# Kernel tuning notes

Hardware: AMD Instinct MI355X
Metric: run time of the kernel (lower is better)

The kernel has to match this reference:

```python
import jax, jax.numpy as jnp
import numpy as np

B, N, K = 2, 8192, 16
D1, D2, OUT = 128, 256, 128


def setup_inputs() -> dict:
    key = jax.random.key(0)
    ks = jax.random.split(key, 6)
    return {
        "xyz1": jax.random.normal(ks[0], (B, N, 3), dtype=jnp.float32),
        "xyz2": jax.random.normal(ks[1], (B, N, 3), dtype=jnp.float32),
        "points1": jax.random.normal(ks[2], (B, N, D1), dtype=jnp.float32),
        "points2": jax.random.normal(ks[3], (B, N, D2), dtype=jnp.float32),
        # Conv1d(k=1) == pointwise linear: weight [OUT, D1+D2], bias [OUT]
        "W": jax.random.normal(ks[4], (OUT, D1 + D2), dtype=jnp.float32) / np.sqrt(D1 + D2).astype(np.float32),
        "b": jax.random.normal(ks[5], (OUT,), dtype=jnp.float32) * 0.01,
        "nsample": K,
    }


def reference(xyz1, xyz2, points1, points2, W, b, nsample):
    Bb, Nn, _ = xyz1.shape
    # squared pairwise distances, queries=xyz2, keys=xyz1 -> [B, N, N]
    d2 = (jnp.sum(xyz2 * xyz2, -1)[:, :, None]
          + jnp.sum(xyz1 * xyz1, -1)[:, None, :]
          - 2.0 * jnp.einsum('bsc,bnc->bsn', xyz2, xyz1))
    neg_vals, idx = jax.lax.top_k(-d2, nsample)          # K nearest
    dists = -neg_vals                                     # [B, N, K] sq dists
    recip = 1.0 / (dists + 1e-8)
    weight = recip / jnp.sum(recip, axis=2, keepdims=True)  # inverse-dist weights
    # gather neighbor features from points2: [B, N, K, D2]
    g = jnp.take_along_axis(points2, idx.reshape(Bb, Nn * nsample)[:, :, None], axis=1)
    g = g.reshape(Bb, Nn, nsample, -1)
    interp = jnp.sum(g * weight[..., None], axis=2)       # [B, N, D2]
    cat = jnp.concatenate([points1, interp], axis=-1)     # [B, N, D1+D2]
    # Conv1d(kernel=1) over channel dim
    return jnp.einsum('bnc,oc->bno', cat, W) + b
```

## Files before the change

### kernel.cpp

```cpp
#include <hip/hip_runtime.h>
#include <stdint.h>

#define BQ   2
#define NQ   8192
#define D1Q  128
#define D2Q  256
#define OUTQ 128
#define CATQ 384
#define KQ   16

#define NBIN 4096
#define RED_MARGIN 1e-3f
#define LB_MARGIN  1e-2f

#define WS_WFH   0
#define WS_WFL   98304
#define WS_HIST  196608
#define WS_SPXYZ 262144
#define WS_QSXYZ 524288
#define WS_SPIDX 786432
#define WS_QSIDX 819200
#define WS_GBLO  851968
#define WS_GBHI  856064

__device__ __forceinline__ ushort f2bf(float f) {
    uint32_t u = __float_as_uint(f);
    return (ushort)((u + 0x7FFFu + ((u >> 16) & 1u)) >> 16);
}
__device__ __forceinline__ float bf2f(ushort h) {
    return __uint_as_float((uint32_t)h << 16);
}

typedef __attribute__((ext_vector_type(8))) short short8v;
typedef __attribute__((ext_vector_type(4))) float f32x4v;

__device__ __forceinline__ int mort_bin(float x, float y, float z) {
    int bx = (int)((x + 5.0f) * 1.6f); bx = bx < 0 ? 0 : (bx > 15 ? 15 : bx);
    int by = (int)((y + 5.0f) * 1.6f); by = by < 0 ? 0 : (by > 15 ? 15 : by);
    int bz = (int)((z + 5.0f) * 1.6f); bz = bz < 0 ? 0 : (bz > 15 ? 15 : bz);
    int k = 0;
    #pragma unroll
    for (int t = 0; t < 4; ++t)
        k |= (((bx >> t) & 1) << (3 * t)) | (((by >> t) & 1) << (3 * t + 1)) |
             (((bz >> t) & 1) << (3 * t + 2));
    return k;
}

__global__ void prep_w_kernel(const float* __restrict__ W,
                              ushort* __restrict__ Wfh, ushort* __restrict__ Wfl,
                              uint32_t* __restrict__ hist) {
    int flat = blockIdx.x * 256 + threadIdx.x;
    if (flat < CATQ * OUTQ) {
        int r    = flat & 7;
        int lane = (flat >> 3) & 63;
        int ctk  = flat >> 9;
        int ct   = ctk & 7;
        int kt   = ctk >> 3;
        int o = ct * 16 + (lane & 15);
        int k = kt * 32 + (lane >> 4) * 8 + r;
        float v  = W[o * CATQ + k];
        ushort h = f2bf(v);
        Wfh[flat] = h;
        Wfl[flat] = f2bf(v - bf2f(h));
    }
    if (flat < 4 * NBIN) hist[flat] = 0u;
}

__global__ void hist_kernel(const float* __restrict__ xyz1,
                            const float* __restrict__ xyz2,
                            uint32_t* __restrict__ hist) {
    int i = blockIdx.x * 256 + threadIdx.x;
    if (i < BQ * NQ) {
        int batch = i >> 13;
        const float* p = xyz1 + (size_t)i * 3;
        int bin = mort_bin(p[0], p[1], p[2]);
        atomicAdd(&hist[batch * NBIN + bin], 1u);
    } else {
        int j = i - BQ * NQ;
        int batch = j >> 13;
        const float* p = xyz2 + (size_t)j * 3;
        int bin = mort_bin(p[0], p[1], p[2]);
        atomicAdd(&hist[(2 + batch) * NBIN + bin], 1u);
    }
}

__global__ void prefix_kernel(uint32_t* __restrict__ hist) {
    __shared__ uint32_t sc[1024];
    uint32_t* h = hist + (size_t)blockIdx.x * NBIN;
    int t = threadIdx.x;
    uint32_t v0 = h[4 * t], v1 = h[4 * t + 1], v2 = h[4 * t + 2], v3 = h[4 * t + 3];
    uint32_t s = v0 + v1 + v2 + v3;
    sc[t] = s;
    __syncthreads();
    for (int d = 1; d < 1024; d <<= 1) {
        uint32_t x = (t >= d) ? sc[t - d] : 0u;
        __syncthreads();
        sc[t] += x;
        __syncthreads();
    }
    uint32_t excl = sc[t] - s;
    h[4 * t]     = excl;
    h[4 * t + 1] = excl + v0;
    h[4 * t + 2] = excl + v0 + v1;
    h[4 * t + 3] = excl + v0 + v1 + v2;
}

__global__ void scatter_kernel(const float* __restrict__ xyz1,
                               const float* __restrict__ xyz2,
                               uint32_t* __restrict__ hist,
                               float4* __restrict__ sp_xyzn,
                               float4* __restrict__ qs_xyzw,
                               ushort* __restrict__ sp_idx,
                               ushort* __restrict__ qs_idx) {
    int i = blockIdx.x * 256 + threadIdx.x;
    if (i < BQ * NQ) {
        int batch = i >> 13;
        const float* p = xyz1 + (size_t)i * 3;
        float x = p[0], y = p[1], z = p[2];
        int bin = mort_bin(x, y, z);
        uint32_t pos = atomicAdd(&hist[batch * NBIN + bin], 1u);
        float n;
        {
            #pragma clang fp contract(off)
            float px = x * x, py = y * y, pz = z * z;
            n = (px + py) + pz;
        }
        sp_xyzn[batch * NQ + pos] = make_float4(x, y, z, n);
        sp_idx[batch * NQ + pos]  = (ushort)(i & (NQ - 1));
    } else {
        int j = i - BQ * NQ;
        int batch = j >> 13;
        const float* p = xyz2 + (size_t)j * 3;
        float x = p[0], y = p[1], z = p[2];
        int bin = mort_bin(x, y, z);
        uint32_t pos = atomicAdd(&hist[(2 + batch) * NBIN + bin], 1u);
        float s2;
        {
            #pragma clang fp contract(off)
            float px = x * x, py = y * y, pz = z * z;
            s2 = (px + py) + pz;
        }
        qs_xyzw[batch * NQ + pos] = make_float4(x, y, z, s2);
        qs_idx[batch * NQ + pos]  = (ushort)(j & (NQ - 1));
    }
}

__global__ void gbox_kernel(const float4* __restrict__ sp_xyzn,
                            float4* __restrict__ gblo, float4* __restrict__ gbhi) {
    int g = blockIdx.x;
    int lane = threadIdx.x;
    float4 pt = sp_xyzn[(size_t)g * 64 + lane];
    float lx = pt.x, ly = pt.y, lz = pt.z;
    float hx = pt.x, hy = pt.y, hz = pt.z;
    #pragma unroll
    for (int d = 1; d < 64; d <<= 1) {
        lx = fminf(lx, __shfl_xor(lx, d, 64));
        ly = fminf(ly, __shfl_xor(ly, d, 64));
        lz = fminf(lz, __shfl_xor(lz, d, 64));
        hx = fmaxf(hx, __shfl_xor(hx, d, 64));
        hy = fmaxf(hy, __shfl_xor(hy, d, 64));
        hz = fmaxf(hz, __shfl_xor(hz, d, 64));
    }
    if (lane == 0) {
        gblo[g] = make_float4(lx, ly, lz, 0.f);
        gbhi[g] = make_float4(hx, hy, hz, 0.f);
    }
}

__device__ __forceinline__ float npy_d2(float4 pt, float qx, float qy, float qz,
                                        float s2) {
    #pragma clang fp contract(off)
    float d0  = pt.x * qx;
    float dot = fmaf(pt.y, qy, d0);
    dot       = fmaf(pt.z, qz, dot);
    float tt  = s2 + pt.w;
    return tt - 2.0f * dot;
}

__device__ __forceinline__ float red_r(float4 pt, float qx, float qy, float qz) {
    float dot = fmaf(pt.z, qz, fmaf(pt.y, qy, pt.x * qx));
    return fmaf(-2.0f, dot, pt.w);
}

__device__ __forceinline__ uint64_t sort64(uint64_t x, int lane) {
    #pragma unroll
    for (int k = 2; k <= 64; k <<= 1) {
        #pragma unroll
        for (int j = k >> 1; j > 0; j >>= 1) {
            uint64_t p = __shfl_xor((unsigned long long)x, j, 64);
            bool keep_min = (((lane & j) == 0) == ((lane & k) == 0));
            bool pless    = p < x;
            x = (pless == keep_min) ? p : x;
        }
    }
    return x;
}

__global__ __launch_bounds__(256, 4) void fused_kernel(
        const float4* __restrict__ sp_xyzn, const ushort* __restrict__ sp_idx,
        const float4* __restrict__ qs_xyzw, const ushort* __restrict__ qs_idx,
        const float* __restrict__ points1, const float* __restrict__ points2,
        const ushort* __restrict__ Wfh, const ushort* __restrict__ Wfl,
        const float* __restrict__ bias,
        const float4* __restrict__ gblo, const float4* __restrict__ gbhi,
        float* __restrict__ out) {
    __shared__ __align__(16) char smem[33792];
    float4*   xyzt4 = (float4*)smem;
    uint64_t* wball = (uint64_t*)(smem + 16384);
    ushort*   pidm  = (ushort*)(smem + 32768);
    ushort*   slist = (ushort*)(smem + 33280);
    ushort*   qsl   = (ushort*)(smem + 33536);
    uint32_t* scntp = (uint32_t*)(smem + 33568);
    float4*   qbl   = (float4*)(smem + 33584);
    float4*   qbh   = (float4*)(smem + 33648);
    float*    thmaxA= (float*)(smem + 33712);
    ushort*   cat_h = (ushort*)smem;
    ushort*   cat_l = (ushort*)(smem + 12544);

    const int tid   = threadIdx.x;
    const int lane  = tid & 63;
    const int w     = tid >> 6;
    const int blk   = blockIdx.x;
    const int b     = blk >> 9;
    const int qslot = (blk & 511) * 16;

    if (tid == 0) *scntp = 0u;
    if (tid < 16) qsl[tid] = qs_idx[b * NQ + qslot + tid];

    float qx[4], qy[4], qz[4], s2[4];
    int   oqi[4];
    #pragma unroll
    for (int j = 0; j < 4; ++j) {
        float4 q = qs_xyzw[(size_t)b * NQ + qslot + w * 4 + j];
        qx[j] = q.x; qy[j] = q.y; qz[j] = q.z; s2[j] = q.w;
        oqi[j] = (int)qs_idx[b * NQ + qslot + w * 4 + j];
    }
    {
        float blx = qx[0], bly = qy[0], blz = qz[0];
        float bhx = qx[0], bhy = qy[0], bhz = qz[0];
        #pragma unroll
        for (int j = 1; j < 4; ++j) {
            blx = fminf(blx, qx[j]); bly = fminf(bly, qy[j]); blz = fminf(blz, qz[j]);
            bhx = fmaxf(bhx, qx[j]); bhy = fmaxf(bhy, qy[j]); bhz = fmaxf(bhz, qz[j]);
        }
        if (lane == 0) {
            qbl[w] = make_float4(blx, bly, blz, 0.f);
            qbh[w] = make_float4(bhx, bhy, bhz, 0.f);
        }
    }

    const float4* spb = sp_xyzn + (size_t)b * NQ;
    const ushort* spi = sp_idx  + (size_t)b * NQ;

    int wstart = qslot + 8 - 1024;
    if (wstart < 0) wstart = 0;
    if (wstart > NQ - 2048) wstart = NQ - 2048;
    wstart &= ~63;

    float mn[4];
    #pragma unroll
    for (int j = 0; j < 4; ++j) mn[j] = __uint_as_float(0x7F800000u);

    for (int tile = 0; tile < 2; ++tile) {
        __syncthreads();
        {
            const float4* s4 = spb + wstart + tile * 1024;
            #pragma unroll
            for (int v = tid; v < 1024; v += 256) xyzt4[v] = s4[v];
        }
        __syncthreads();
        #pragma unroll 4
        for (int s = 0; s < 16; ++s) {
            float4 pt = xyzt4[s * 64 + lane];
            #pragma unroll
            for (int j = 0; j < 4; ++j)
                mn[j] = fminf(mn[j], red_r(pt, qx[j], qy[j], qz[j]));
        }
    }

    float that[4];
    #pragma unroll
    for (int j = 0; j < 4; ++j) {
        float x = mn[j];
        #pragma unroll
        for (int k = 2; k <= 64; k <<= 1) {
            #pragma unroll
            for (int jj = k >> 1; jj > 0; jj >>= 1) {
                float px = __shfl_xor(x, jj, 64);
                bool keep_min = (((lane & jj) == 0) == ((lane & k) == 0));
                float mnv = fminf(x, px), mxv = fmaxf(x, px);
                x = keep_min ? mnv : mxv;
            }
        }
        that[j] = s2[j] + __shfl(x, 15, 64) + RED_MARGIN;
    }
    {
        float tm = fmaxf(fmaxf(that[0], that[1]), fmaxf(that[2], that[3]));
        if (lane == 0) thmaxA[w] = tm;
    }
    __syncthreads();

    if (tid < 128) {
        float4 gl = gblo[b * 128 + tid];
        float4 gh = gbhi[b * 128 + tid];
        float qlx = fminf(fminf(qbl[0].x, qbl[1].x), fminf(qbl[2].x, qbl[3].x));
        float qly = fminf(fminf(qbl[0].y, qbl[1].y), fminf(qbl[2].y, qbl[3].y));
        float qlz = fminf(fminf(qbl[0].z, qbl[1].z), fminf(qbl[2].z, qbl[3].z));
        float qhx = fmaxf(fmaxf(qbh[0].x, qbh[1].x), fmaxf(qbh[2].x, qbh[3].x));
        float qhy = fmaxf(fmaxf(qbh[0].y, qbh[1].y), fmaxf(qbh[2].y, qbh[3].y));
        float qhz = fmaxf(fmaxf(qbh[0].z, qbh[1].z), fmaxf(qbh[2].z, qbh[3].z));
        float tmax = fmaxf(fmaxf(thmaxA[0], thmaxA[1]),
                           fmaxf(thmaxA[2], thmaxA[3]));
        float dx = fmaxf(fmaxf(qlx - gh.x, gl.x - qhx), 0.f);
        float dy = fmaxf(fmaxf(qly - gh.y, gl.y - qhy), 0.f);
        float dz = fmaxf(fmaxf(qlz - gh.z, gl.z - qhz), 0.f);
        float lb = dx * dx;
        lb = fmaf(dy, dy, lb);
        lb = fmaf(dz, dz, lb);
        if (lb <= tmax + LB_MARGIN) {
            uint32_t p = atomicAdd(scntp, 1u);
            slist[p] = (ushort)tid;
        }
    }
    __syncthreads();
    const int scnt = (int)*scntp;

    uint32_t cnt[4] = {0u, 0u, 0u, 0u};
    for (int c0 = 0; c0 < scnt; c0 += 4) {
        __syncthreads();
        {
            int which = c0 + (tid >> 6);
            if (which < scnt) {
                int off = (int)slist[which] * 64 + (tid & 63);
                xyzt4[tid] = spb[off];
                pidm[tid]  = spi[off];
            }
        }
        __syncthreads();
        const int nch = (scnt - c0) < 4 ? (scnt - c0) : 4;
        for (int k = 0; k < nch; ++k) {
            float4 pt = xyzt4[k * 64 + lane];
            #pragma unroll
            for (int j = 0; j < 4; ++j) {
                float d2 = npy_d2(pt, qx[j], qy[j], qz[j], s2[j]);
                bool  v  = (d2 <= that[j]);
                uint64_t mask = __ballot((int)v);
                if (mask != 0ull) {
                    if (v) {
                        uint32_t below = __builtin_amdgcn_mbcnt_hi(
                            (uint32_t)(mask >> 32),
                            __builtin_amdgcn_mbcnt_lo((uint32_t)mask, 0u));
                        uint32_t pos    = cnt[j] + below;
                        uint32_t bits   = __float_as_uint(d2);
                        uint32_t mapped = bits ^ (0x80000000u |
                                          (uint32_t)((int32_t)bits >> 31));
                        if (pos < 128u) {
                            uint32_t pidx = (uint32_t)pidm[k * 64 + lane];
                            wball[(w * 4 + j) * 128 + pos] =
                                ((uint64_t)mapped << 32) | (uint64_t)pidx;
                        }
                    }
                    cnt[j] += (uint32_t)__popcll(mask);
                }
            }
        }
    }

    int   myidxA[4];
    float mywgtA[4];
    #pragma unroll
    for (int j = 0; j < 4; ++j) {
        const uint64_t* wb = wball + (size_t)(w * 4 + j) * 128;
        const uint32_t c = cnt[j];
        uint64_t mykey;
        if (c <= 64u) {
            uint64_t k0 = (lane < (int)c) ? wb[lane] : ~0ull;
            mykey = sort64(k0, lane);
        } else {
            uint32_t cc = c > 128u ? 128u : c;
            uint64_t k0 = wb[lane];
            uint64_t k1 = (lane + 64 < (int)cc) ? wb[lane + 64] : ~0ull;
            k0 = sort64(k0, lane);
            k1 = sort64(k1, lane);
            uint64_t t1 = __shfl((unsigned long long)k1, lane & 15, 64);
            uint64_t km = (lane < 16) ? k0 : ((lane < 32) ? t1 : ~0ull);
            mykey = sort64(km, lane);
        }
        uint32_t mhi   = (uint32_t)(mykey >> 32);
        uint32_t rbits = (mhi & 0x80000000u) ? (mhi ^ 0x80000000u) : ~mhi;
        float    d2w   = __uint_as_float(rbits);
        myidxA[j] = (int)(uint32_t)(mykey & 0xFFFFFFFFull);
        float recip = (lane < KQ) ? (1.0f / (d2w + 1e-8f)) : 0.0f;
        float tot = recip;
        #pragma unroll
        for (int sh = 1; sh < 16; sh <<= 1) tot += __shfl_xor(tot, sh, 64);
        mywgtA[j] = recip / tot;
    }

    __syncthreads();

    const float* p2b = points2 + (size_t)b * NQ * D2Q;
    #pragma unroll
    for (int j = 0; j < 4; ++j) {
        const int qi = w * 4 + j;
        if (lane < 32) {
            float4 p = ((const float4*)(points1 +
                        (size_t)(b * NQ + oqi[j]) * D1Q))[lane];
            ushort4 hv, lv;
            hv.x = f2bf(p.x); lv.x = f2bf(p.x - bf2f(hv.x));
            hv.y = f2bf(p.y); lv.y = f2bf(p.y - bf2f(hv.y));
            hv.z = f2bf(p.z); lv.z = f2bf(p.z - bf2f(hv.z));
            hv.w = f2bf(p.w); lv.w = f2bf(p.w - bf2f(hv.w));
            *(ushort4*)&cat_h[qi * 392 + lane * 4] = hv;
            *(ushort4*)&cat_l[qi * 392 + lane * 4] = lv;
        }
        float4 acc = make_float4(0.f, 0.f, 0.f, 0.f);
        #pragma unroll
        for (int k = 0; k < KQ; ++k) {
            int   kk = __builtin_amdgcn_readlane(myidxA[j], k);
            float wk = __uint_as_float((uint32_t)__builtin_amdgcn_readlane(
                           (int)__float_as_uint(mywgtA[j]), k));
            float4 row = ((const float4*)(p2b + (size_t)kk * D2Q))[lane];
            acc.x = fmaf(wk, row.x, acc.x);
            acc.y = fmaf(wk, row.y, acc.y);
            acc.z = fmaf(wk, row.z, acc.z);
            acc.w = fmaf(wk, row.w, acc.w);
        }
        {
            ushort4 hv, lv;
            hv.x = f2bf(acc.x); lv.x = f2bf(acc.x - bf2f(hv.x));
            hv.y = f2bf(acc.y); lv.y = f2bf(acc.y - bf2f(hv.y));
            hv.z = f2bf(acc.z); lv.z = f2bf(acc.z - bf2f(hv.z));
            hv.w = f2bf(acc.w); lv.w = f2bf(acc.w - bf2f(hv.w));
            *(ushort4*)&cat_h[qi * 392 + D1Q + lane * 4] = hv;
            *(ushort4*)&cat_l[qi * 392 + D1Q + lane * 4] = lv;
        }
    }
    __syncthreads();

    {
        const int arow = lane & 15;
        const int koff = (lane >> 4) * 8;
        const int ct0  = w * 2;
        f32x4v acc0 = {0.f, 0.f, 0.f, 0.f};
        f32x4v acc1 = {0.f, 0.f, 0.f, 0.f};
        #pragma unroll 4
        for (int kt = 0; kt < 12; ++kt) {
            short8v ah = *(const short8v*)&cat_h[arow * 392 + kt * 32 + koff];
            short8v al = *(const short8v*)&cat_l[arow * 392 + kt * 32 + koff];
            const ushort* bhp = Wfh + ((size_t)(kt * 8 + ct0) * 64 + lane) * 8;
            const ushort* blp = Wfl + ((size_t)(kt * 8 + ct0) * 64 + lane) * 8;
            short8v bh0 = *(const short8v*)bhp;
            short8v bl0 = *(const short8v*)blp;
            short8v bh1 = *(const short8v*)(bhp + 512);
            short8v bl1 = *(const short8v*)(blp + 512);
            acc0 = __builtin_amdgcn_mfma_f32_16x16x32_bf16(ah, bh0, acc0, 0, 0, 0);
            acc0 = __builtin_amdgcn_mfma_f32_16x16x32_bf16(al, bh0, acc0, 0, 0, 0);
            acc0 = __builtin_amdgcn_mfma_f32_16x16x32_bf16(ah, bl0, acc0, 0, 0, 0);
            acc1 = __builtin_amdgcn_mfma_f32_16x16x32_bf16(ah, bh1, acc1, 0, 0, 0);
            acc1 = __builtin_amdgcn_mfma_f32_16x16x32_bf16(al, bh1, acc1, 0, 0, 0);
            acc1 = __builtin_amdgcn_mfma_f32_16x16x32_bf16(ah, bl1, acc1, 0, 0, 0);
        }
        const int col0   = ct0 * 16 + (lane & 15);
        const int r0slot = (lane >> 4) * 4;
        const float bv0 = bias[col0];
        const float bv1 = bias[col0 + 16];
        #pragma unroll
        for (int r = 0; r < 4; ++r) {
            int oq = (int)qsl[r0slot + r];
            size_t rowoff = (size_t)(b * NQ + oq) * OUTQ;
            out[rowoff + col0]      = acc0[r] + bv0;
            out[rowoff + col0 + 16] = acc1[r] + bv1;
        }
    }
}

extern "C" void kernel_launch(void* const* d_in, const int* in_sizes, int n_in,
                              void* d_out, int out_size, void* d_ws, size_t ws_size,
                              hipStream_t stream) {
    const float* xyz1    = (const float*)d_in[0];
    const float* xyz2    = (const float*)d_in[1];
    const float* points1 = (const float*)d_in[2];
    const float* points2 = (const float*)d_in[3];
    const float* W       = (const float*)d_in[4];
    const float* bias    = (const float*)d_in[5];

    char* ws = (char*)d_ws;
    ushort*   Wfh     = (ushort*)(ws + WS_WFH);
    ushort*   Wfl     = (ushort*)(ws + WS_WFL);
    uint32_t* hist    = (uint32_t*)(ws + WS_HIST);
    float4*   sp_xyzn = (float4*)(ws + WS_SPXYZ);
    float4*   qs_xyzw = (float4*)(ws + WS_QSXYZ);
    ushort*   sp_idx  = (ushort*)(ws + WS_SPIDX);
    ushort*   qs_idx  = (ushort*)(ws + WS_QSIDX);
    float4*   gblo    = (float4*)(ws + WS_GBLO);
    float4*   gbhi    = (float4*)(ws + WS_GBHI);

    prep_w_kernel<<<192, 256, 0, stream>>>(W, Wfh, Wfl, hist);
    hist_kernel<<<128, 256, 0, stream>>>(xyz1, xyz2, hist);
    prefix_kernel<<<4, 1024, 0, stream>>>(hist);
    scatter_kernel<<<128, 256, 0, stream>>>(xyz1, xyz2, hist,
                                            sp_xyzn, qs_xyzw, sp_idx, qs_idx);
    gbox_kernel<<<256, 64, 0, stream>>>(sp_xyzn, gblo, gbhi);
    fused_kernel<<<(BQ * NQ) / 16, 256, 0, stream>>>(
        sp_xyzn, sp_idx, qs_xyzw, qs_idx, points1, points2,
        Wfh, Wfl, bias, gblo, gbhi, (float*)d_out);
}
```

Baseline: 164.3 us.

## Fold group boxes into scatter and make kNN candidate search per-wave

```diff
diff --git a/kernel.cpp b/kernel.cpp
--- a/kernel.cpp
+++ b/kernel.cpp
@@ -20,8 +20,7 @@
 #define WS_QSXYZ 524288
 #define WS_SPIDX 786432
 #define WS_QSIDX 819200
-#define WS_GBLO  851968
-#define WS_GBHI  856064
+#define WS_GB    851968
 
 __device__ __forceinline__ ushort f2bf(float f) {
     uint32_t u = __float_as_uint(f);
@@ -29,6 +28,20 @@
 }
 __device__ __forceinline__ float bf2f(ushort h) {
     return __uint_as_float((uint32_t)h << 16);
+}
+
+__device__ __forceinline__ uint32_t encf(float f) {
+    uint32_t b = __float_as_uint(f);
+    return b ^ (0x80000000u | (uint32_t)((int32_t)b >> 31));
+}
+__device__ __forceinline__ float decf(uint32_t u) {
+    uint32_t bits = (u & 0x80000000u) ? (u ^ 0x80000000u) : ~u;
+    return __uint_as_float(bits);
+}
+
+__device__ __forceinline__ uint32_t mbcnt64(uint64_t m) {
+    return __builtin_amdgcn_mbcnt_hi((uint32_t)(m >> 32),
+           __builtin_amdgcn_mbcnt_lo((uint32_t)m, 0u));
 }
 
 typedef __attribute__((ext_vector_type(8))) short short8v;
@@ -48,7 +61,8 @@
 
 __global__ void prep_w_kernel(const float* __restrict__ W,
                               ushort* __restrict__ Wfh, ushort* __restrict__ Wfl,
-                              uint32_t* __restrict__ hist) {
+                              uint32_t* __restrict__ hist,
+                              uint32_t* __restrict__ gbU) {
     int flat = blockIdx.x * 256 + threadIdx.x;
     if (flat < CATQ * OUTQ) {
         int r    = flat & 7;
@@ -64,6 +78,7 @@
         Wfl[flat] = f2bf(v - bf2f(h));
     }
     if (flat < 4 * NBIN) hist[flat] = 0u;
+    if (flat < 256 * 8)  gbU[flat] = ((flat & 7) >= 4) ? 0u : 0xFFFFFFFFu;
 }
 
 __global__ void hist_kernel(const float* __restrict__ xyz1,
@@ -111,7 +126,8 @@
                                float4* __restrict__ sp_xyzn,
                                float4* __restrict__ qs_xyzw,
                                ushort* __restrict__ sp_idx,
-                               ushort* __restrict__ qs_idx) {
+                               ushort* __restrict__ qs_idx,
+                               uint32_t* __restrict__ gbU) {
     int i = blockIdx.x * 256 + threadIdx.x;
     if (i < BQ * NQ) {
         int batch = i >> 13;
@@ -127,6 +143,13 @@
         }
         sp_xyzn[batch * NQ + pos] = make_float4(x, y, z, n);
         sp_idx[batch * NQ + pos]  = (ushort)(i & (NQ - 1));
+        uint32_t* gw = gbU + ((size_t)batch * 128 + (pos >> 6)) * 8;
+        atomicMin(&gw[0], encf(x));
+        atomicMin(&gw[1], encf(y));
+        atomicMin(&gw[2], encf(z));
+        atomicMax(&gw[4], encf(x));
+        atomicMax(&gw[5], encf(y));
+        atomicMax(&gw[6], encf(z));
     } else {
         int j = i - BQ * NQ;
         int batch = j >> 13;
@@ -145,28 +168,6 @@
     }
 }
 
-__global__ void gbox_kernel(const float4* __restrict__ sp_xyzn,
-                            float4* __restrict__ gblo, float4* __restrict__ gbhi) {
-    int g = blockIdx.x;
-    int lane = threadIdx.x;
-    float4 pt = sp_xyzn[(size_t)g * 64 + lane];
-    float lx = pt.x, ly = pt.y, lz = pt.z;
-    float hx = pt.x, hy = pt.y, hz = pt.z;
-    #pragma unroll
-    for (int d = 1; d < 64; d <<= 1) {
-        lx = fminf(lx, __shfl_xor(lx, d, 64));
-        ly = fminf(ly, __shfl_xor(ly, d, 64));
-        lz = fminf(lz, __shfl_xor(lz, d, 64));
-        hx = fmaxf(hx, __shfl_xor(hx, d, 64));
-        hy = fmaxf(hy, __shfl_xor(hy, d, 64));
-        hz = fmaxf(hz, __shfl_xor(hz, d, 64));
-    }
-    if (lane == 0) {
-        gblo[g] = make_float4(lx, ly, lz, 0.f);
-        gbhi[g] = make_float4(hx, hy, hz, 0.f);
-    }
-}
-
 __device__ __forceinline__ float npy_d2(float4 pt, float qx, float qy, float qz,
                                         float s2) {
     #pragma clang fp contract(off)
@@ -201,21 +202,14 @@
         const float4* __restrict__ qs_xyzw, const ushort* __restrict__ qs_idx,
         const float* __restrict__ points1, const float* __restrict__ points2,
         const ushort* __restrict__ Wfh, const ushort* __restrict__ Wfl,
-        const float* __restrict__ bias,
-        const float4* __restrict__ gblo, const float4* __restrict__ gbhi,
+        const float* __restrict__ bias, const uint32_t* __restrict__ gbU,
         float* __restrict__ out) {
-    __shared__ __align__(16) char smem[33792];
-    float4*   xyzt4 = (float4*)smem;
-    uint64_t* wball = (uint64_t*)(smem + 16384);
-    ushort*   pidm  = (ushort*)(smem + 32768);
-    ushort*   slist = (ushort*)(smem + 33280);
-    ushort*   qsl   = (ushort*)(smem + 33536);
-    uint32_t* scntp = (uint32_t*)(smem + 33568);
-    float4*   qbl   = (float4*)(smem + 33584);
-    float4*   qbh   = (float4*)(smem + 33648);
-    float*    thmaxA= (float*)(smem + 33712);
+    __shared__ __align__(16) char smem[26368];
+    uint64_t* wball = (uint64_t*)smem;
     ushort*   cat_h = (ushort*)smem;
     ushort*   cat_l = (ushort*)(smem + 12544);
+    ushort*   slist = (ushort*)(smem + 25088);
+    ushort*   qsl   = (ushort*)(smem + 26112);
 
     const int tid   = threadIdx.x;
     const int lane  = tid & 63;
@@ -224,7 +218,6 @@
     const int b     = blk >> 9;
     const int qslot = (blk & 511) * 16;
 
-    if (tid == 0) *scntp = 0u;
     if (tid < 16) qsl[tid] = qs_idx[b * NQ + qslot + tid];
 
     float qx[4], qy[4], qz[4], s2[4];
@@ -235,47 +228,26 @@
         qx[j] = q.x; qy[j] = q.y; qz[j] = q.z; s2[j] = q.w;
         oqi[j] = (int)qs_idx[b * NQ + qslot + w * 4 + j];
     }
-    {
-        float blx = qx[0], bly = qy[0], blz = qz[0];
-        float bhx = qx[0], bhy = qy[0], bhz = qz[0];
-        #pragma unroll
-        for (int j = 1; j < 4; ++j) {
-            blx = fminf(blx, qx[j]); bly = fminf(bly, qy[j]); blz = fminf(blz, qz[j]);
-            bhx = fmaxf(bhx, qx[j]); bhy = fmaxf(bhy, qy[j]); bhz = fmaxf(bhz, qz[j]);
-        }
-        if (lane == 0) {
-            qbl[w] = make_float4(blx, bly, blz, 0.f);
-            qbh[w] = make_float4(bhx, bhy, bhz, 0.f);
-        }
-    }
 
     const float4* spb = sp_xyzn + (size_t)b * NQ;
     const ushort* spi = sp_idx  + (size_t)b * NQ;
 
-    int wstart = qslot + 8 - 1024;
+    int wstart = qslot + 8 - 512;
     if (wstart < 0) wstart = 0;
-    if (wstart > NQ - 2048) wstart = NQ - 2048;
+    if (wstart > NQ - 1024) wstart = NQ - 1024;
     wstart &= ~63;
+    const float4* win = spb + wstart;
 
     float mn[4];
     #pragma unroll
     for (int j = 0; j < 4; ++j) mn[j] = __uint_as_float(0x7F800000u);
 
-    for (int tile = 0; tile < 2; ++tile) {
-        __syncthreads();
-        {
-            const float4* s4 = spb + wstart + tile * 1024;
-            #pragma unroll
-            for (int v = tid; v < 1024; v += 256) xyzt4[v] = s4[v];
-        }
-        __syncthreads();
-        #pragma unroll 4
-        for (int s = 0; s < 16; ++s) {
-            float4 pt = xyzt4[s * 64 + lane];
-            #pragma unroll
-            for (int j = 0; j < 4; ++j)
-                mn[j] = fminf(mn[j], red_r(pt, qx[j], qy[j], qz[j]));
-        }
+    #pragma unroll 4
+    for (int s = 0; s < 16; ++s) {
+        float4 pt = win[s * 64 + lane];
+        #pragma unroll
+        for (int j = 0; j < 4; ++j)
+            mn[j] = fminf(mn[j], red_r(pt, qx[j], qy[j], qz[j]));
     }
 
     float that[4];
@@ -294,74 +266,58 @@
         }
         that[j] = s2[j] + __shfl(x, 15, 64) + RED_MARGIN;
     }
+
+    ushort* sl = slist + w * 128;
+    int scnt_w = 0;
     {
-        float tm = fmaxf(fmaxf(that[0], that[1]), fmaxf(that[2], that[3]));
-        if (lane == 0) thmaxA[w] = tm;
-    }
-    __syncthreads();
-
-    if (tid < 128) {
-        float4 gl = gblo[b * 128 + tid];
-        float4 gh = gbhi[b * 128 + tid];
-        float qlx = fminf(fminf(qbl[0].x, qbl[1].x), fminf(qbl[2].x, qbl[3].x));
-        float qly = fminf(fminf(qbl[0].y, qbl[1].y), fminf(qbl[2].y, qbl[3].y));
-        float qlz = fminf(fminf(qbl[0].z, qbl[1].z), fminf(qbl[2].z, qbl[3].z));
-        float qhx = fmaxf(fmaxf(qbh[0].x, qbh[1].x), fmaxf(qbh[2].x, qbh[3].x));
-        float qhy = fmaxf(fmaxf(qbh[0].y, qbh[1].y), fmaxf(qbh[2].y, qbh[3].y));
-        float qhz = fmaxf(fmaxf(qbh[0].z, qbh[1].z), fmaxf(qbh[2].z, qbh[3].z));
-        float tmax = fmaxf(fmaxf(thmaxA[0], thmaxA[1]),
-                           fmaxf(thmaxA[2], thmaxA[3]));
-        float dx = fmaxf(fmaxf(qlx - gh.x, gl.x - qhx), 0.f);
-        float dy = fmaxf(fmaxf(qly - gh.y, gl.y - qhy), 0.f);
-        float dz = fmaxf(fmaxf(qlz - gh.z, gl.z - qhz), 0.f);
-        float lb = dx * dx;
-        lb = fmaf(dy, dy, lb);
-        lb = fmaf(dz, dz, lb);
-        if (lb <= tmax + LB_MARGIN) {
-            uint32_t p = atomicAdd(scntp, 1u);
-            slist[p] = (ushort)tid;
-        }
-    }
-    __syncthreads();
-    const int scnt = (int)*scntp;
+        float qlx = fminf(fminf(qx[0], qx[1]), fminf(qx[2], qx[3]));
+        float qly = fminf(fminf(qy[0], qy[1]), fminf(qy[2], qy[3]));
+        float qlz = fminf(fminf(qz[0], qz[1]), fminf(qz[2], qz[3]));
+        float qhx = fmaxf(fmaxf(qx[0], qx[1]), fmaxf(qx[2], qx[3]));
+        float qhy = fmaxf(fmaxf(qy[0], qy[1]), fmaxf(qy[2], qy[3]));
+        float qhz = fmaxf(fmaxf(qz[0], qz[1]), fmaxf(qz[2], qz[3]));
+        float tmax = fmaxf(fmaxf(that[0], that[1]), fmaxf(that[2], that[3]))
+                   + LB_MARGIN;
+        #pragma unroll
+        for (int h = 0; h < 2; ++h) {
+            int g = h * 64 + lane;
+            const uint32_t* gw = gbU + ((size_t)b * 128 + g) * 8;
+            float glx = decf(gw[0]), gly = decf(gw[1]), glz = decf(gw[2]);
+            float ghx = decf(gw[4]), ghy = decf(gw[5]), ghz = decf(gw[6]);
+            float dx = fmaxf(fmaxf(qlx - ghx, glx - qhx), 0.f);
+            float dy = fmaxf(fmaxf(qly - ghy, gly - qhy), 0.f);
+            float dz = fmaxf(fmaxf(qlz - ghz, glz - qhz), 0.f);
+            float lb = dx * dx;
+            lb = fmaf(dy, dy, lb);
+            lb = fmaf(dz, dz, lb);
+            bool sv = (lb <= tmax);
+            uint64_t m = __ballot((int)sv);
+            if (sv) sl[scnt_w + mbcnt64(m)] = (ushort)g;
+            scnt_w += (int)__popcll(m);
+        }
+    }
 
     uint32_t cnt[4] = {0u, 0u, 0u, 0u};
-    for (int c0 = 0; c0 < scnt; c0 += 4) {
-        __syncthreads();
-        {
-            int which = c0 + (tid >> 6);
-            if (which < scnt) {
-                int off = (int)slist[which] * 64 + (tid & 63);
-                xyzt4[tid] = spb[off];
-                pidm[tid]  = spi[off];
-            }
-        }
-        __syncthreads();
-        const int nch = (scnt - c0) < 4 ? (scnt - c0) : 4;
-        for (int k = 0; k < nch; ++k) {
-            float4 pt = xyzt4[k * 64 + lane];
-            #pragma unroll
-            for (int j = 0; j < 4; ++j) {
-                float d2 = npy_d2(pt, qx[j], qy[j], qz[j], s2[j]);
-                bool  v  = (d2 <= that[j]);
-                uint64_t mask = __ballot((int)v);
-                if (mask != 0ull) {
-                    if (v) {
-                        uint32_t below = __builtin_amdgcn_mbcnt_hi(
-                            (uint32_t)(mask >> 32),
-                            __builtin_amdgcn_mbcnt_lo((uint32_t)mask, 0u));
-                        uint32_t pos    = cnt[j] + below;
-                        uint32_t bits   = __float_as_uint(d2);
-                        uint32_t mapped = bits ^ (0x80000000u |
-                                          (uint32_t)((int32_t)bits >> 31));
-                        if (pos < 128u) {
-                            uint32_t pidx = (uint32_t)pidm[k * 64 + lane];
-                            wball[(w * 4 + j) * 128 + pos] =
-                                ((uint64_t)mapped << 32) | (uint64_t)pidx;
-                        }
-                    }
-                    cnt[j] += (uint32_t)__popcll(mask);
+    for (int i = 0; i < scnt_w; ++i) {
+        const int g = (int)sl[i];
+        float4   pt   = spb[g * 64 + lane];
+        uint32_t pidx = (uint32_t)spi[g * 64 + lane];
+        #pragma unroll
+        for (int j = 0; j < 4; ++j) {
+            float d2 = npy_d2(pt, qx[j], qy[j], qz[j], s2[j]);
+            bool  v  = (d2 <= that[j]);
+            uint64_t mask = __ballot((int)v);
+            if (mask != 0ull) {
+                if (v) {
+                    uint32_t pos    = cnt[j] + mbcnt64(mask);
+                    uint32_t bits   = __float_as_uint(d2);
+                    uint32_t mapped = bits ^ (0x80000000u |
+                                      (uint32_t)((int32_t)bits >> 31));
+                    if (pos < 128u)
+                        wball[(w * 4 + j) * 128 + pos] =
+                            ((uint64_t)mapped << 32) | (uint64_t)pidx;
                 }
+                cnt[j] += (uint32_t)__popcll(mask);
             }
         }
     }
@@ -493,16 +449,14 @@
     float4*   qs_xyzw = (float4*)(ws + WS_QSXYZ);
     ushort*   sp_idx  = (ushort*)(ws + WS_SPIDX);
     ushort*   qs_idx  = (ushort*)(ws + WS_QSIDX);
-    float4*   gblo    = (float4*)(ws + WS_GBLO);
-    float4*   gbhi    = (float4*)(ws + WS_GBHI);
-
-    prep_w_kernel<<<192, 256, 0, stream>>>(W, Wfh, Wfl, hist);
+    uint32_t* gbU     = (uint32_t*)(ws + WS_GB);
+
+    prep_w_kernel<<<192, 256, 0, stream>>>(W, Wfh, Wfl, hist, gbU);
     hist_kernel<<<128, 256, 0, stream>>>(xyz1, xyz2, hist);
     prefix_kernel<<<4, 1024, 0, stream>>>(hist);
     scatter_kernel<<<128, 256, 0, stream>>>(xyz1, xyz2, hist,
-                                            sp_xyzn, qs_xyzw, sp_idx, qs_idx);
-    gbox_kernel<<<256, 64, 0, stream>>>(sp_xyzn, gblo, gbhi);
+                                            sp_xyzn, qs_xyzw, sp_idx, qs_idx, gbU);
     fused_kernel<<<(BQ * NQ) / 16, 256, 0, stream>>>(
         sp_xyzn, sp_idx, qs_xyzw, qs_idx, points1, points2,
-        Wfh, Wfl, bias, gblo, gbhi, (float*)d_out);
-}
+        Wfh, Wfl, bias, gbU, (float*)d_out);
+}
```

After: 179.2 us. 9.0% more time.
